# Kernel optimization log

Hardware: AMD Instinct MI355X
Metric: run time of the kernel (lower is better)

Reference implementation:

```python
import jax, jax.numpy as jnp
import numpy as np

B, D_IN, N, L, P, C = 512, 784, 2048, 6, 15, 10  # batch, input, width, dag layers, weight pairs, classes


def setup_inputs() -> dict:
    key = jax.random.key(0)
    ks = jax.random.split(key, 10)
    x = jax.random.normal(ks[0], (B, D_IN), jnp.float32)
    w_in = jax.random.normal(ks[1], (N, D_IN), jnp.float32) * 0.1
    b_in = jax.random.normal(ks[2], (N,), jnp.float32) * 0.1
    W = jax.random.normal(ks[3], (P, N, N), jnp.float32) * 0.1
    # binary 0/1 float masks standing in for DAG connectivity masks
    M = jax.random.bernoulli(ks[4], 0.5, (P, N, N)).astype(jnp.float32)
    b = jax.random.normal(ks[5], (L - 1, N), jnp.float32) * 0.1
    w_out1 = jax.random.normal(ks[6], (C, N), jnp.float32) * 0.1
    b_out1 = jax.random.normal(ks[7], (C,), jnp.float32) * 0.1
    w_out2 = jax.random.normal(ks[8], (C, N), jnp.float32) * 0.1
    b_out2 = jax.random.normal(ks[9], (C,), jnp.float32) * 0.1
    return {"x": x, "w_in": w_in, "b_in": b_in, "W": W, "M": M, "b": b,
            "w_out1": w_out1, "b_out1": b_out1, "w_out2": w_out2, "b_out2": b_out2}


def reference(x, w_in, b_in, W, M, b, w_out1, b_out1, w_out2, b_out2):
    # input layer
    acts = [jax.nn.relu(x @ w_in.T + b_in)]  # [B, N]
    idx = 0
    for i in range(1, L):  # DAG layer i has predecessors 0..i-1
        Wm = W[idx:idx + i] * M[idx:idx + i]          # [i, N, N] masked weights
        stacked = jnp.stack(acts)                      # [i, B, N]
        # sum over predecessors of inp @ Wm.T; bias added once per predecessor
        out = jnp.einsum('jbn,jmn->bm', stacked, Wm) + i * b[i - 1]
        acts.append(jax.nn.relu(out))
        idx += i
    return acts[-1] @ w_out1.T + b_out1 + acts[-2] @ w_out2.T + b_out2
```

## Files before the change

kernel.cpp:

```cpp
#include <hip/hip_runtime.h>

typedef __bf16 bf16;
typedef __attribute__((ext_vector_type(8))) __bf16 bf16x8;
typedef __attribute__((ext_vector_type(4))) __bf16 bf16x4;
typedef __attribute__((ext_vector_type(4))) float floatx4;

#define B_SZ 512
#define N_SZ 2048
#define DIN  784
#define DINP 800
#define ACT_LD 12288

__device__ __forceinline__ void load_lds16(const bf16* g, bf16* l) {
    __builtin_amdgcn_global_load_lds(
        (const __attribute__((address_space(1))) void*)g,
        (__attribute__((address_space(3))) void*)l, 16, 0, 0);
}

__global__ __launch_bounds__(256)
void prep_kernel(const float* __restrict__ x, const float* __restrict__ w_in,
                 bf16* __restrict__ xb, bf16* __restrict__ w_inb)
{
    int g = blockIdx.x * 256 + threadIdx.x;
    const int GPR = DINP / 4;
    const float* src; bf16* dst; int row, c;
    if (g < B_SZ * GPR) {
        row = g / GPR; c = g - row * GPR;
        src = x + (size_t)row * DIN;  dst = xb + (size_t)row * DINP;
    } else {
        int h = g - B_SZ * GPR;
        row = h / GPR; c = h - row * GPR;
        src = w_in + (size_t)row * DIN;  dst = w_inb + (size_t)row * DINP;
    }
    int k = c * 4;
    floatx4 v = (floatx4){0.f, 0.f, 0.f, 0.f};
    if (k < DIN) v = *(const floatx4*)(src + k);
    bf16x4 o;
    o[0] = (bf16)v[0]; o[1] = (bf16)v[1]; o[2] = (bf16)v[2]; o[3] = (bf16)v[3];
    *(bf16x4*)(dst + k) = o;
}

__global__ __launch_bounds__(256, 2)
void gemm_kernel(const bf16* __restrict__ A, int lda,
                 const bf16* __restrict__ Bm, int ldb,
                 float* __restrict__ partial,
                 int chunkK, int Ktot)
{
    __shared__ bf16 As[128 * 32];
    __shared__ bf16 Bs[128 * 32];

    const int t    = threadIdx.x;
    const int lane = t & 63, wave = t >> 6;
    const int wm   = (wave & 1) * 64, wn = (wave >> 1) * 64;
    const int l15  = lane & 15, quad = lane >> 4;
    const int n0   = blockIdx.x * 128, m0 = blockIdx.y * 128;
    const int s    = blockIdx.z;
    const int kb   = s * chunkK;
    const int ke   = (kb + chunkK < Ktot) ? (kb + chunkK) : Ktot;

    const int rA = wave * 16 + (lane >> 2);
    const int cA = (lane & 3) * 8;
    const bf16* pA0 = A  + (size_t)(m0 + rA) * lda + cA + kb;
    const bf16* pA1 = pA0 + (size_t)64 * lda;
    const bf16* pB0 = Bm + (size_t)(n0 + rA) * ldb + cA + kb;
    const bf16* pB1 = pB0 + (size_t)64 * ldb;
    bf16* dA0 = &As[wave * 512];  bf16* dA1 = &As[(wave + 4) * 512];
    bf16* dB0 = &Bs[wave * 512];  bf16* dB1 = &Bs[(wave + 4) * 512];

    floatx4 acc[4][4];
#pragma unroll
    for (int a = 0; a < 4; a++)
#pragma unroll
        for (int b = 0; b < 4; b++) acc[a][b] = (floatx4){0.f, 0.f, 0.f, 0.f};

    for (int k0 = kb; k0 < ke; k0 += 32) {
        __syncthreads();
        load_lds16(pA0, dA0);  load_lds16(pA1, dA1);
        load_lds16(pB0, dB0);  load_lds16(pB1, dB1);
        pA0 += 32; pA1 += 32; pB0 += 32; pB1 += 32;
        __syncthreads();

        bf16x8 af[4], bfr[4];
#pragma unroll
        for (int a = 0; a < 4; a++)
            af[a] = *(const bf16x8*)(&As[(wm + a * 16 + l15) * 32 + quad * 8]);
#pragma unroll
        for (int b = 0; b < 4; b++)
            bfr[b] = *(const bf16x8*)(&Bs[(wn + b * 16 + l15) * 32 + quad * 8]);
#pragma unroll
        for (int a = 0; a < 4; a++)
#pragma unroll
            for (int b = 0; b < 4; b++)
                acc[a][b] = __builtin_amdgcn_mfma_f32_16x16x32_bf16(af[a], bfr[b], acc[a][b], 0, 0, 0);
    }

    float* outp = partial + (size_t)s * (B_SZ * N_SZ);
#pragma unroll
    for (int a = 0; a < 4; a++)
#pragma unroll
        for (int b = 0; b < 4; b++)
#pragma unroll
            for (int r = 0; r < 4; r++) {
                int row = m0 + wm + a * 16 + quad * 4 + r;
                int col = n0 + wn + b * 16 + l15;
                outp[(size_t)row * N_SZ + col] = acc[a][b][r];
            }
}

__global__ __launch_bounds__(256, 2)
void dag_gemm_kernel(const bf16* __restrict__ A,
                     const float* __restrict__ Wl, const float* __restrict__ Ml,
                     float* __restrict__ partial,
                     int chunkK)
{
    __shared__ bf16 As[2][256 * 32];
    __shared__ bf16 Bs[2][64 * 32];

    const int t    = threadIdx.x;
    const int lane = t & 63, wave = t >> 6;
    const int l15  = lane & 15, quad = lane >> 4;
    const int n0   = blockIdx.x * 64, m0 = blockIdx.y * 256;
    const int kb   = blockIdx.z * chunkK;
    const int ke   = kb + chunkK;

    const int ar = wave * 16 + (lane >> 2);
    const int ac = (lane & 3) * 8;
    const int br = t >> 2, bc = (t & 3) * 8;
    const size_t wrow = (size_t)(n0 + br) << 11;

    floatx4 acc[4][4];
#pragma unroll
    for (int a = 0; a < 4; a++)
#pragma unroll
        for (int b = 0; b < 4; b++) acc[a][b] = (floatx4){0.f, 0.f, 0.f, 0.f};

    bf16x8 a0, a1, a2, a3;
    floatx4 wv0, wv1, mv0, mv1;

    auto load_regs = [&](int k) {
        const bf16* ap = A + (size_t)(m0 + ar) * ACT_LD + k + ac;
        a0 = *(const bf16x8*)(ap);
        a1 = *(const bf16x8*)(ap + (size_t)64  * ACT_LD);
        a2 = *(const bf16x8*)(ap + (size_t)128 * ACT_LD);
        a3 = *(const bf16x8*)(ap + (size_t)192 * ACT_LD);
        int jj = k >> 11, kk = k & 2047;
        size_t o = ((size_t)jj << 22) + wrow + kk + bc;
        wv0 = *(const floatx4*)(Wl + o);  wv1 = *(const floatx4*)(Wl + o + 4);
        mv0 = *(const floatx4*)(Ml + o);  mv1 = *(const floatx4*)(Ml + o + 4);
    };

    auto do_step = [&](int buf, int knext, bool pref) {
        bf16x8 o8;
        o8[0] = (bf16)(wv0[0] * mv0[0]); o8[1] = (bf16)(wv0[1] * mv0[1]);
        o8[2] = (bf16)(wv0[2] * mv0[2]); o8[3] = (bf16)(wv0[3] * mv0[3]);
        o8[4] = (bf16)(wv1[0] * mv1[0]); o8[5] = (bf16)(wv1[1] * mv1[1]);
        o8[6] = (bf16)(wv1[2] * mv1[2]); o8[7] = (bf16)(wv1[3] * mv1[3]);
        *(bf16x8*)(&Bs[buf][br * 32 + bc]) = o8;
        *(bf16x8*)(&As[buf][(ar +   0) * 32 + ac]) = a0;
        *(bf16x8*)(&As[buf][(ar +  64) * 32 + ac]) = a1;
        *(bf16x8*)(&As[buf][(ar + 128) * 32 + ac]) = a2;
        *(bf16x8*)(&As[buf][(ar + 192) * 32 + ac]) = a3;
        if (pref) load_regs(knext);
        __syncthreads();
        bf16x8 af[4], bfr[4];
#pragma unroll
        for (int a = 0; a < 4; a++)
            af[a] = *(const bf16x8*)(&As[buf][(wave * 64 + a * 16 + l15) * 32 + quad * 8]);
#pragma unroll
        for (int b = 0; b < 4; b++)
            bfr[b] = *(const bf16x8*)(&Bs[buf][(b * 16 + l15) * 32 + quad * 8]);
#pragma unroll
        for (int a = 0; a < 4; a++)
#pragma unroll
            for (int b = 0; b < 4; b++)
                acc[a][b] = __builtin_amdgcn_mfma_f32_16x16x32_bf16(af[a], bfr[b], acc[a][b], 0, 0, 0);
    };

    load_regs(kb);
    for (int k0 = kb; k0 < ke; k0 += 64) {
        do_step(0, k0 + 32, true);
        do_step(1, k0 + 64, (k0 + 64) < ke);
    }

    float* outp = partial + (size_t)blockIdx.z * (B_SZ * N_SZ);
#pragma unroll
    for (int a = 0; a < 4; a++)
#pragma unroll
        for (int b = 0; b < 4; b++)
#pragma unroll
            for (int r = 0; r < 4; r++) {
                int row = m0 + wave * 64 + a * 16 + quad * 4 + r;
                int col = n0 + b * 16 + l15;
                outp[(size_t)row * N_SZ + col] = acc[a][b][r];
            }
}

__global__ __launch_bounds__(256)
void epilogue_kernel(const float* __restrict__ partial, int S,
                     const float* __restrict__ bias, float bscale,
                     bf16* __restrict__ actdst)
{
    int g = blockIdx.x * 256 + threadIdx.x;
    size_t off = (size_t)g * 4;
    int b = (int)(off >> 11);
    int n = (int)(off & (N_SZ - 1));
    floatx4 v = *(const floatx4*)(partial + off);
    for (int s2 = 1; s2 < S; s2++)
        v += *(const floatx4*)(partial + (size_t)s2 * (B_SZ * N_SZ) + off);
    floatx4 bv = *(const floatx4*)(bias + n);
    bf16x4 o;
#pragma unroll
    for (int j = 0; j < 4; j++) {
        float xv = v[j] + bscale * bv[j];
        xv = xv > 0.f ? xv : 0.f;
        o[j] = (bf16)xv;
    }
    *(bf16x4*)(actdst + (size_t)b * ACT_LD + n) = o;
}

__global__ __launch_bounds__(64)
void out_kernel(const bf16* __restrict__ act4, const bf16* __restrict__ act5,
                const float* __restrict__ w1, const float* __restrict__ b1,
                const float* __restrict__ w2, const float* __restrict__ b2,
                float* __restrict__ out)
{
    int b = blockIdx.x, lane = threadIdx.x;
    float a5[32], a4[32];
#pragma unroll
    for (int rep = 0; rep < 4; rep++) {
        bf16x8 v5 = *(const bf16x8*)(act5 + (size_t)b * ACT_LD + rep * 512 + lane * 8);
        bf16x8 v4 = *(const bf16x8*)(act4 + (size_t)b * ACT_LD + rep * 512 + lane * 8);
#pragma unroll
        for (int j = 0; j < 8; j++) {
            a5[rep * 8 + j] = (float)v5[j];
            a4[rep * 8 + j] = (float)v4[j];
        }
    }
    for (int c = 0; c < 10; c++) {
        float d = 0.f;
#pragma unroll
        for (int rep = 0; rep < 4; rep++) {
            floatx4 wa = *(const floatx4*)(w1 + (size_t)c * N_SZ + rep * 512 + lane * 8);
            floatx4 wb = *(const floatx4*)(w1 + (size_t)c * N_SZ + rep * 512 + lane * 8 + 4);
            floatx4 va = *(const floatx4*)(w2 + (size_t)c * N_SZ + rep * 512 + lane * 8);
            floatx4 vb = *(const floatx4*)(w2 + (size_t)c * N_SZ + rep * 512 + lane * 8 + 4);
#pragma unroll
            for (int j = 0; j < 4; j++) {
                d += a5[rep * 8 + j] * wa[j] + a4[rep * 8 + j] * va[j];
                d += a5[rep * 8 + 4 + j] * wb[j] + a4[rep * 8 + 4 + j] * vb[j];
            }
        }
        for (int off = 32; off > 0; off >>= 1) d += __shfl_down(d, off);
        if (lane == 0) out[b * 10 + c] = d + b1[c] + b2[c];
    }
}

extern "C" void kernel_launch(void* const* d_in, const int* in_sizes, int n_in,
                              void* d_out, int out_size, void* d_ws, size_t ws_size,
                              hipStream_t stream)
{
    const float* x    = (const float*)d_in[0];
    const float* w_in = (const float*)d_in[1];
    const float* b_in = (const float*)d_in[2];
    const float* W    = (const float*)d_in[3];
    const float* M    = (const float*)d_in[4];
    const float* bL   = (const float*)d_in[5];
    const float* w1   = (const float*)d_in[6];
    const float* b1   = (const float*)d_in[7];
    const float* w2   = (const float*)d_in[8];
    const float* b2   = (const float*)d_in[9];
    float* out = (float*)d_out;

    char* ws = (char*)d_ws;
    bf16*  xb      = (bf16*)ws;
    bf16*  w_inb   = (bf16*)(ws + 819200);
    bf16*  actsT   = (bf16*)(ws + 4096000);
    float* partial = (float*)(ws + 16678912);

    prep_kernel<<<2000, 256, 0, stream>>>(x, w_in, xb, w_inb);

    gemm_kernel<<<dim3(16, 4, 4), 256, 0, stream>>>(
        xb, DINP, w_inb, DINP, partial, 224, DINP);
    epilogue_kernel<<<1024, 256, 0, stream>>>(partial, 4, b_in, 1.0f, actsT);

    for (int i = 1; i < 6; i++) {
        int idx = i * (i - 1) / 2;
        const float* Wl = W + ((size_t)idx << 22);
        const float* Ml = M + ((size_t)idx << 22);
        dag_gemm_kernel<<<dim3(32, 2, 8), 256, 0, stream>>>(
            actsT, Wl, Ml, partial, 256 * i);
        epilogue_kernel<<<1024, 256, 0, stream>>>(
            partial, 8, bL + (size_t)(i - 1) * N_SZ, (float)i,
            actsT + (size_t)i * N_SZ);
    }

    out_kernel<<<512, 64, 0, stream>>>(
        actsT + (size_t)4 * N_SZ, actsT + (size_t)5 * N_SZ,
        w1, b1, w2, b2, out);
}
```

Before: 691.5 us.

## Cover full batch per block in DAG GEMM so masked weights load once

Retiles the DAG GEMM so each 512-thread block covers all 512 batch rows with a 32-column weight tile, instead of 256 rows by 64 columns. The fp32 weight and mask matrices, the dominant memory traffic, are then read once rather than once per batch half. In exchange, weight loads become narrower (2 floats per thread) and the bf16 activation tile is re-read by twice as many column blocks, with a larger LDS footprint.

```diff
diff --git a/kernel.cpp b/kernel.cpp
--- a/kernel.cpp
+++ b/kernel.cpp
@@ -3,7 +3,9 @@
 typedef __bf16 bf16;
 typedef __attribute__((ext_vector_type(8))) __bf16 bf16x8;
 typedef __attribute__((ext_vector_type(4))) __bf16 bf16x4;
+typedef __attribute__((ext_vector_type(2))) __bf16 bf16x2;
 typedef __attribute__((ext_vector_type(4))) float floatx4;
+typedef __attribute__((ext_vector_type(2))) float floatx2;
 
 #define B_SZ 512
 #define N_SZ 2048
@@ -107,72 +109,69 @@
             }
 }
 
-__global__ __launch_bounds__(256, 2)
+__global__ __launch_bounds__(512, 4)
 void dag_gemm_kernel(const bf16* __restrict__ A,
                      const float* __restrict__ Wl, const float* __restrict__ Ml,
                      float* __restrict__ partial,
                      int chunkK)
 {
-    __shared__ bf16 As[2][256 * 32];
-    __shared__ bf16 Bs[2][64 * 32];
+    __shared__ bf16 As[2][512 * 32];
+    __shared__ bf16 Bs[2][32 * 32];
 
     const int t    = threadIdx.x;
     const int lane = t & 63, wave = t >> 6;
     const int l15  = lane & 15, quad = lane >> 4;
-    const int n0   = blockIdx.x * 64, m0 = blockIdx.y * 256;
+    const int n0   = blockIdx.x * 32;
     const int kb   = blockIdx.z * chunkK;
     const int ke   = kb + chunkK;
 
-    const int ar = wave * 16 + (lane >> 2);
-    const int ac = (lane & 3) * 8;
-    const int br = t >> 2, bc = (t & 3) * 8;
-    const size_t wrow = (size_t)(n0 + br) << 11;
-
-    floatx4 acc[4][4];
-#pragma unroll
-    for (int a = 0; a < 4; a++)
-#pragma unroll
-        for (int b = 0; b < 4; b++) acc[a][b] = (floatx4){0.f, 0.f, 0.f, 0.f};
+    const int ar = t >> 2, ac = (t & 3) * 8;
+    const int brow = t >> 4, bk = (t & 15) * 2;
+    const size_t wbase = (size_t)(n0 + brow) << 11;
+
+    floatx4 acc[4][2];
+#pragma unroll
+    for (int a = 0; a < 4; a++)
+#pragma unroll
+        for (int b = 0; b < 2; b++) acc[a][b] = (floatx4){0.f, 0.f, 0.f, 0.f};
 
     bf16x8 a0, a1, a2, a3;
-    floatx4 wv0, wv1, mv0, mv1;
+    floatx2 wv, mv;
 
     auto load_regs = [&](int k) {
-        const bf16* ap = A + (size_t)(m0 + ar) * ACT_LD + k + ac;
+        const bf16* ap = A + (size_t)ar * ACT_LD + k + ac;
         a0 = *(const bf16x8*)(ap);
-        a1 = *(const bf16x8*)(ap + (size_t)64  * ACT_LD);
-        a2 = *(const bf16x8*)(ap + (size_t)128 * ACT_LD);
-        a3 = *(const bf16x8*)(ap + (size_t)192 * ACT_LD);
+        a1 = *(const bf16x8*)(ap + (size_t)128 * ACT_LD);
+        a2 = *(const bf16x8*)(ap + (size_t)256 * ACT_LD);
+        a3 = *(const bf16x8*)(ap + (size_t)384 * ACT_LD);
         int jj = k >> 11, kk = k & 2047;
-        size_t o = ((size_t)jj << 22) + wrow + kk + bc;
-        wv0 = *(const floatx4*)(Wl + o);  wv1 = *(const floatx4*)(Wl + o + 4);
-        mv0 = *(const floatx4*)(Ml + o);  mv1 = *(const floatx4*)(Ml + o + 4);
+        size_t o = ((size_t)jj << 22) + wbase + kk + bk;
+        wv = *(const floatx2*)(Wl + o);
+        mv = *(const floatx2*)(Ml + o);
     };
 
     auto do_step = [&](int buf, int knext, bool pref) {
-        bf16x8 o8;
-        o8[0] = (bf16)(wv0[0] * mv0[0]); o8[1] = (bf16)(wv0[1] * mv0[1]);
-        o8[2] = (bf16)(wv0[2] * mv0[2]); o8[3] = (bf16)(wv0[3] * mv0[3]);
-        o8[4] = (bf16)(wv1[0] * mv1[0]); o8[5] = (bf16)(wv1[1] * mv1[1]);
-        o8[6] = (bf16)(wv1[2] * mv1[2]); o8[7] = (bf16)(wv1[3] * mv1[3]);
-        *(bf16x8*)(&Bs[buf][br * 32 + bc]) = o8;
+        bf16x2 pp;
+        pp[0] = (bf16)(wv[0] * mv[0]);
+        pp[1] = (bf16)(wv[1] * mv[1]);
+        *(bf16x2*)(&Bs[buf][brow * 32 + bk]) = pp;
         *(bf16x8*)(&As[buf][(ar +   0) * 32 + ac]) = a0;
-        *(bf16x8*)(&As[buf][(ar +  64) * 32 + ac]) = a1;
-        *(bf16x8*)(&As[buf][(ar + 128) * 32 + ac]) = a2;
-        *(bf16x8*)(&As[buf][(ar + 192) * 32 + ac]) = a3;
+        *(bf16x8*)(&As[buf][(ar + 128) * 32 + ac]) = a1;
+        *(bf16x8*)(&As[buf][(ar + 256) * 32 + ac]) = a2;
+        *(bf16x8*)(&As[buf][(ar + 384) * 32 + ac]) = a3;
         if (pref) load_regs(knext);
         __syncthreads();
-        bf16x8 af[4], bfr[4];
+        bf16x8 af[4], bfr[2];
 #pragma unroll
         for (int a = 0; a < 4; a++)
             af[a] = *(const bf16x8*)(&As[buf][(wave * 64 + a * 16 + l15) * 32 + quad * 8]);
 #pragma unroll
-        for (int b = 0; b < 4; b++)
+        for (int b = 0; b < 2; b++)
             bfr[b] = *(const bf16x8*)(&Bs[buf][(b * 16 + l15) * 32 + quad * 8]);
 #pragma unroll
         for (int a = 0; a < 4; a++)
 #pragma unroll
-            for (int b = 0; b < 4; b++)
+            for (int b = 0; b < 2; b++)
                 acc[a][b] = __builtin_amdgcn_mfma_f32_16x16x32_bf16(af[a], bfr[b], acc[a][b], 0, 0, 0);
     };
 
@@ -186,10 +185,10 @@
 #pragma unroll
     for (int a = 0; a < 4; a++)
 #pragma unroll
-        for (int b = 0; b < 4; b++)
+        for (int b = 0; b < 2; b++)
 #pragma unroll
             for (int r = 0; r < 4; r++) {
-                int row = m0 + wave * 64 + a * 16 + quad * 4 + r;
+                int row = wave * 64 + a * 16 + quad * 4 + r;
                 int col = n0 + b * 16 + l15;
                 outp[(size_t)row * N_SZ + col] = acc[a][b][r];
             }
@@ -287,7 +286,7 @@
         int idx = i * (i - 1) / 2;
         const float* Wl = W + ((size_t)idx << 22);
         const float* Ml = M + ((size_t)idx << 22);
-        dag_gemm_kernel<<<dim3(32, 2, 8), 256, 0, stream>>>(
+        dag_gemm_kernel<<<dim3(64, 1, 8), 512, 0, stream>>>(
             actsT, Wl, Ml, partial, 256 * i);
         epilogue_kernel<<<1024, 256, 0, stream>>>(
             partial, 8, bL + (size_t)(i - 1) * N_SZ, (float)i,
```

New measurement: 767.0 us. 10.9% more time.
